# Kernel tuning notes

Measured on AMD Instinct MI355X. Metric: run time of the kernel, lower is better.

The kernel has to match this reference:

```python
import jax, jax.numpy as jnp
import numpy as np

BATCH = 256
B_TYPES = 32   # input capsule types
C_TYPES = 10   # output capsule types
H, W = 8, 8    # input spatial extent == kernel (output is 1x1)
POSE = 16      # capsule pose length (shape (16,1))
NUM_ITER = 3
EPS = 1e-8


def setup_inputs() -> dict:
    key = jax.random.key(0)
    k1, k2, k3 = jax.random.split(key, 3)
    input_caps_poses = jax.random.normal(k1, (BATCH, B_TYPES, H, W, POSE, 1), jnp.float32)
    input_caps_activations = jax.random.uniform(k2, (BATCH, B_TYPES, H, W), jnp.float32)
    # nn.init.normal_(std=0.1) on [B, kh, kw, C, os0, is0]
    weight = 0.1 * jax.random.normal(k3, (B_TYPES, H, W, C_TYPES, POSE, POSE), jnp.float32)
    # routing_bias initialized to 0.1: [C, oh, ow, os0, os1]
    routing_bias = jnp.full((C_TYPES, 1, 1, POSE, 1), 0.1, jnp.float32)
    return {
        "input_caps_poses": input_caps_poses,
        "input_caps_activations": input_caps_activations,
        "weight": weight,
        "routing_bias": routing_bias,
    }


def _squash(s):
    # Hinton squash: ||s||^2/(1+||s||^2) * s/||s||, norm over pose dims
    n2 = jnp.sum(s * s, axis=(-2, -1), keepdims=True)
    return (n2 / (1.0 + n2)) * s * jax.lax.rsqrt(n2 + EPS)


def reference(input_caps_poses, input_caps_activations, weight, routing_bias):
    b = input_caps_poses.shape[0]
    # votes[b,c,B,h,w,o,p] = sum_i W[B,h,w,c,o,i] * pose[b,B,h,w,i,p]
    votes = jnp.einsum('Bhwcoi,bBhwip->bcBhwop', weight, input_caps_poses)
    logits = jnp.zeros((b, C_TYPES, B_TYPES, H, W), votes.dtype)
    bias = routing_bias.reshape(1, C_TYPES, POSE, 1)
    v = None
    for it in range(NUM_ITER):
        # coupling coefficients: softmax over output capsule types
        c = jax.nn.softmax(logits, axis=1)                      # [b,C,B,h,w]
        # weighted sum of votes over all input capsules (B,h,w)
        s = jnp.einsum('bcBhw,bcBhwop->bcop', c, votes) + bias  # [b,C,16,1]
        v = _squash(s)
        if it < NUM_ITER - 1:
            # agreement: dot(vote, output pose)
            logits = logits + jnp.einsum('bcBhwop,bcop->bcBhw', votes, v)
    output_caps_poses = v[:, :, None, None, :, :]               # [b,C,1,1,16,1]
    output_caps_activations = jnp.sqrt(
        jnp.sum(v * v, axis=(-2, -1)) + EPS)[:, :, None, None]  # [b,C,1,1]
    return output_caps_poses, output_caps_activations
```

## Files before the change

### kernel.cpp

```cpp
#include <hip/hip_runtime.h>
#include <hip/hip_fp16.h>
#include <math.h>


typedef _Float16 f16;
typedef _Float16 f16x2 __attribute__((ext_vector_type(2)));
typedef _Float16 f16x4 __attribute__((ext_vector_type(4)));
typedef _Float16 f16x8 __attribute__((ext_vector_type(8)));
typedef __fp16   h16x2 __attribute__((ext_vector_type(2)));
typedef float f32x4 __attribute__((ext_vector_type(4)));

#define DPP_ADD(v, ctrl) ((v) + __int_as_float(__builtin_amdgcn_update_dpp( \
    0, __float_as_int(v), (ctrl), 0xF, 0xF, true)))

__device__ __forceinline__ f16x2 pk(float a, float b) {
    h16x2 t = __builtin_amdgcn_cvt_pkrtz(a, b);
    return __builtin_bit_cast(f16x2, t);
}

#if __has_builtin(__builtin_amdgcn_fdot2)
__device__ __forceinline__ float FDOT2(f16x2 a, f16x2 b, float c) {
    return __builtin_amdgcn_fdot2(__builtin_bit_cast(h16x2, a),
                                  __builtin_bit_cast(h16x2, b), c, false);
}
#else
__device__ __forceinline__ float FDOT2(f16x2 a, f16x2 b, float c) {
    return c + (float)a[0] * (float)b[0] + (float)a[1] * (float)b[1];
}
#endif

constexpr int WS_ROW = 28;
constexpr int XS_ROW = 76;

__device__ __forceinline__ float xorsum4(float v) {
    v += __shfl_xor(v, 16, 64);
    v += __shfl_xor(v, 32, 64);
    return v;
}

__device__ __forceinline__ f16x4 cvt4(float4 w) {
    f16x2 a = pk(w.x, w.y);
    f16x2 b = pk(w.z, w.w);
    f16x4 r; r[0] = a[0]; r[1] = a[1]; r[2] = b[0]; r[3] = b[1];
    return r;
}

template<int PASS>
__global__ __launch_bounds__(256)
void pass_k(const float* __restrict__ poses, const float* __restrict__ weight,
            const float* __restrict__ bias,
            const float* __restrict__ sp0, const float* __restrict__ sp1,
            float* __restrict__ s_dst)
{
    __shared__ f16 Ws[640 * WS_ROW];
    __shared__ f16 xs[64 * XS_ROW];

    const int tid  = threadIdx.x;
    const int blk  = blockIdx.x;
    const int ngrp = blk >> 2;
    const int b0   = (blk & 3) * 64;
    const int wave = tid >> 6;
    const int lane = tid & 63;
    const int q    = lane >> 4;
    const int lo   = lane & 15;
    const int wtb  = wave * 16;
    const int bg   = b0 + wtb;
    const int nl0  = q >> 1;
    const int iq   = (q & 1) * 8;

    f16x2 vsp[10][2];
    if (PASS >= 1) {
        const int rowb = (bg + lo) * 10;
        #pragma unroll
        for (int c = 0; c < 10; ++c) {
            float4 bb = *(const float4*)(bias + c * 16 + q * 4);
            float4 sa = *(const float4*)(sp0 + (size_t)(rowb + c) * 16 + q * 4);
            float t0 = sa.x + bb.x, t1 = sa.y + bb.y, t2 = sa.z + bb.z, t3 = sa.w + bb.w;
            float n2 = xorsum4(t0*t0 + t1*t1 + t2*t2 + t3*t3);
            float sc = n2 / (1.f + n2) * rsqrtf(n2 + 1e-8f);
            float v0 = sc*t0, v1 = sc*t1, v2 = sc*t2, v3 = sc*t3;
            if (PASS == 2) {
                float4 sb = *(const float4*)(sp1 + (size_t)(rowb + c) * 16 + q * 4);
                float u0 = sb.x + bb.x, u1 = sb.y + bb.y, u2 = sb.z + bb.z, u3 = sb.w + bb.w;
                float m2 = xorsum4(u0*u0 + u1*u1 + u2*u2 + u3*u3);
                float sc2 = m2 / (1.f + m2) * rsqrtf(m2 + 1e-8f);
                v0 += sc2*u0; v1 += sc2*u1; v2 += sc2*u2; v3 += sc2*u3;
            }
            vsp[c][0] = pk(v0, v1);
            vsp[c][1] = pk(v2, v3);
        }
    }

    float4 wreg[10];
    float4 xreg[4];
    const int b_loc = tid >> 2, part = tid & 3;

    auto load_iter = [&](int l) {
        const float* wp = weight + (size_t)(ngrp * 4 + l) * 10240;
        #pragma unroll
        for (int k = 0; k < 10; ++k) wreg[k] = ((const float4*)wp)[tid + k * 256];
        const float* xp = poses + (size_t)(b0 + b_loc) * 32768
                          + (size_t)(ngrp * 16 + l * 4 + part) * 16;
        #pragma unroll
        for (int j = 0; j < 4; ++j) xreg[j] = ((const float4*)xp)[j];
    };
    auto store_iter = [&]() {
        #pragma unroll
        for (int k = 0; k < 10; ++k) {
            const int f = tid + k * 256;
            *(f16x4*)&Ws[(f >> 2) * WS_ROW + (f & 3) * 4] = cvt4(wreg[k]);
        }
        f16* lp = xs + b_loc * XS_ROW + part * 16;
        #pragma unroll
        for (int j = 0; j < 4; ++j) *(f16x4*)&lp[j * 4] = cvt4(xreg[j]);
    };

    f32x4 acc[10];
    #pragma unroll
    for (int c = 0; c < 10; ++c) acc[c] = (f32x4){0.f, 0.f, 0.f, 0.f};

    f16x2 cf[10][2];

    load_iter(0);

    for (int l = 0; l < 4; ++l) {
        __syncthreads();
        store_iter();
        if (l + 1 < 4) load_iter(l + 1);
        __syncthreads();

        if (PASS >= 1) {
            float ce[10];
            #pragma unroll
            for (int n = 0; n < 4; ++n) {
                f16x4 bx = *(const f16x4*)&xs[(wtb + lo) * XS_ROW + n * 16 + q * 4];
                float lg[10];
                #pragma unroll
                for (int c = 0; c < 10; ++c) {
                    f16x4 aw = *(const f16x4*)&Ws[((n * 10 + c) * 16 + lo) * WS_ROW + q * 4];
                    f32x4 D = __builtin_amdgcn_mfma_f32_16x16x16f16(
                        aw, bx, (f32x4){0.f, 0.f, 0.f, 0.f}, 0, 0, 0);
                    float p = FDOT2(pk(D[0], D[1]), vsp[c][0], 0.f);
                    p = FDOT2(pk(D[2], D[3]), vsp[c][1], p);
                    lg[c] = xorsum4(p);
                }
                float m = lg[0];
                #pragma unroll
                for (int c = 1; c < 10; ++c) m = fmaxf(m, lg[c]);
                float sum = 0.f;
                #pragma unroll
                for (int c = 0; c < 10; ++c) { lg[c] = __expf(lg[c] - m); sum += lg[c]; }
                const float inv = 1.f / sum;
                if (n & 1) {
                    #pragma unroll
                    for (int c = 0; c < 10; ++c)
                        cf[c][n >> 1] = pk(ce[c], lg[c] * inv);
                } else {
                    #pragma unroll
                    for (int c = 0; c < 10; ++c) ce[c] = lg[c] * inv;
                }
            }
        }

        f16x8 xa[2];
        #pragma unroll
        for (int np = 0; np < 2; ++np) {
            const f16* p = &xs[(wtb + lo) * XS_ROW + (np * 2 + nl0) * 16 + iq];
            f16x4 x0 = *(const f16x4*)p;
            f16x4 x1 = *(const f16x4*)(p + 4);
            xa[np] = __builtin_shufflevector(x0, x1, 0, 1, 2, 3, 4, 5, 6, 7);
        }
        #pragma unroll
        for (int c = 0; c < 10; ++c) {
            #pragma unroll
            for (int np = 0; np < 2; ++np) {
                f16 ch;
                if (PASS == 0) {
                    ch = (f16)0.1f;
                } else {
                    union { f16x2 h; unsigned u; } cu; cu.h = cf[c][np];
                    unsigned hv = nl0 ? (cu.u >> 16) : (cu.u & 0xffffu);
                    union { unsigned short s; f16 h; } hu; hu.s = (unsigned short)hv;
                    ch = hu.h;
                }
                const int n_loc = np * 2 + nl0;
                const f16* wp_ = &Ws[((n_loc * 10 + c) * 16 + lo) * WS_ROW + iq];
                f16x4 w0 = *(const f16x4*)wp_;
                f16x4 w1 = *(const f16x4*)(wp_ + 4);
                f16x8 bw = __builtin_shufflevector(w0, w1, 0, 1, 2, 3, 4, 5, 6, 7);
                f16x8 av = xa[np] * ch;
                acc[c] = __builtin_amdgcn_mfma_f32_16x16x32_f16(av, bw, acc[c], 0, 0, 0);
            }
        }
    }

    #pragma unroll
    for (int c = 0; c < 10; ++c) {
        float* sp = s_dst + ((size_t)(bg + q * 4) * 10 + c) * 16 + lo;
        unsafeAtomicAdd(sp + 0 * 160, acc[c][0]);
        unsafeAtomicAdd(sp + 1 * 160, acc[c][1]);
        unsafeAtomicAdd(sp + 2 * 160, acc[c][2]);
        unsafeAtomicAdd(sp + 3 * 160, acc[c][3]);
    }
}

__global__ __launch_bounds__(256)
void epi_k(const float* __restrict__ s2, const float* __restrict__ bias,
           float* __restrict__ out)
{
    const int t = blockIdx.x * 256 + threadIdx.x;
    if (t >= 2560) return;
    const int c = t % 10;
    const float* sp = s2 + (size_t)t * 16;
    const float* bp = bias + c * 16;
    float sv[16];
    float n2 = 0.f;
    #pragma unroll
    for (int o = 0; o < 16; ++o) { float v = sp[o] + bp[o]; sv[o] = v; n2 += v * v; }
    const float scale = n2 / (1.f + n2) * rsqrtf(n2 + 1e-8f);
    float a2 = 0.f;
    #pragma unroll
    for (int o = 0; o < 16; ++o) {
        float v = scale * sv[o];
        out[(size_t)t * 16 + o] = v;
        a2 += v * v;
    }
    out[40960 + t] = sqrtf(a2 + 1e-8f);
}

extern "C" void kernel_launch(void* const* d_in, const int* in_sizes, int n_in,
                              void* d_out, int out_size, void* d_ws, size_t ws_size,
                              hipStream_t stream)
{
    const float* poses  = (const float*)d_in[0];
    const float* weight = (const float*)d_in[2];
    const float* bias   = (const float*)d_in[3];
    float* out = (float*)d_out;
    float* s0 = (float*)d_ws;
    float* s1 = s0 + 40960;
    float* s2 = s1 + 40960;

    (void)hipMemsetAsync(d_ws, 0, 3 * 40960 * sizeof(float), stream);

    pass_k<0><<<512, 256, 0, stream>>>(poses, weight, bias, nullptr, nullptr, s0);
    pass_k<1><<<512, 256, 0, stream>>>(poses, weight, bias, s0, nullptr, s1);
    pass_k<2><<<512, 256, 0, stream>>>(poses, weight, bias, s0, s1, s2);
    epi_k<<<10, 256, 0, stream>>>(s2, bias, out);
}
```

Baseline: 204.7 us.

## Reuse vote MFMA results for weighted sum instead of second MFMA pass

The per-position vote tiles computed by the 16x16x16 MFMA are now kept in registers and accumulated directly, each scaled by its coupling coefficient with FMAs. This replaces the separate 16x16x32 MFMA pass that recomputed the same products from shared memory. The agreement reduction packs two logits into an f16x2 before the cross-lane shuffle, halving shuffle count. Launch bounds now request 2 blocks per CU. Risks are reduced precision in the fp16 logit reduction, a changed atomic write layout, and higher register pressure from holding 10 f32x4 vote tiles.

```diff
diff --git a/kernel.cpp b/kernel.cpp
--- a/kernel.cpp
+++ b/kernel.cpp
@@ -6,12 +6,8 @@
 typedef _Float16 f16;
 typedef _Float16 f16x2 __attribute__((ext_vector_type(2)));
 typedef _Float16 f16x4 __attribute__((ext_vector_type(4)));
-typedef _Float16 f16x8 __attribute__((ext_vector_type(8)));
 typedef __fp16   h16x2 __attribute__((ext_vector_type(2)));
 typedef float f32x4 __attribute__((ext_vector_type(4)));
-
-#define DPP_ADD(v, ctrl) ((v) + __int_as_float(__builtin_amdgcn_update_dpp( \
-    0, __float_as_int(v), (ctrl), 0xF, 0xF, true)))
 
 __device__ __forceinline__ f16x2 pk(float a, float b) {
     h16x2 t = __builtin_amdgcn_cvt_pkrtz(a, b);
@@ -35,6 +31,14 @@
 __device__ __forceinline__ float xorsum4(float v) {
     v += __shfl_xor(v, 16, 64);
     v += __shfl_xor(v, 32, 64);
+    return v;
+}
+
+__device__ __forceinline__ f16x2 xorsum4h(f16x2 v) {
+    union { f16x2 h; int i; } u;
+    union { int i; f16x2 h; } w;
+    u.h = v; w.i = __shfl_xor(u.i, 16, 64); v = v + w.h;
+    u.h = v; w.i = __shfl_xor(u.i, 32, 64); v = v + w.h;
     return v;
 }
 
@@ -46,7 +50,7 @@
 }
 
 template<int PASS>
-__global__ __launch_bounds__(256)
+__global__ __launch_bounds__(256, 2)
 void pass_k(const float* __restrict__ poses, const float* __restrict__ weight,
             const float* __restrict__ bias,
             const float* __restrict__ sp0, const float* __restrict__ sp1,
@@ -65,8 +69,6 @@
     const int lo   = lane & 15;
     const int wtb  = wave * 16;
     const int bg   = b0 + wtb;
-    const int nl0  = q >> 1;
-    const int iq   = (q & 1) * 8;
 
     f16x2 vsp[10][2];
     if (PASS >= 1) {
@@ -119,8 +121,6 @@
     #pragma unroll
     for (int c = 0; c < 10; ++c) acc[c] = (f32x4){0.f, 0.f, 0.f, 0.f};
 
-    f16x2 cf[10][2];
-
     load_iter(0);
 
     for (int l = 0; l < 4; ++l) {
@@ -129,20 +129,30 @@
         if (l + 1 < 4) load_iter(l + 1);
         __syncthreads();
 
-        if (PASS >= 1) {
-            float ce[10];
+        #pragma unroll
+        for (int n = 0; n < 4; ++n) {
+            f16x4 bx = *(const f16x4*)&xs[(wtb + lo) * XS_ROW + n * 16 + q * 4];
+            f32x4 V[10];
             #pragma unroll
-            for (int n = 0; n < 4; ++n) {
-                f16x4 bx = *(const f16x4*)&xs[(wtb + lo) * XS_ROW + n * 16 + q * 4];
+            for (int c = 0; c < 10; ++c) {
+                f16x4 aw = *(const f16x4*)&Ws[((n * 10 + c) * 16 + lo) * WS_ROW + q * 4];
+                V[c] = __builtin_amdgcn_mfma_f32_16x16x16f16(
+                    aw, bx, (f32x4){0.f, 0.f, 0.f, 0.f}, 0, 0, 0);
+            }
+
+            float cfv[10];
+            if (PASS >= 1) {
                 float lg[10];
                 #pragma unroll
-                for (int c = 0; c < 10; ++c) {
-                    f16x4 aw = *(const f16x4*)&Ws[((n * 10 + c) * 16 + lo) * WS_ROW + q * 4];
-                    f32x4 D = __builtin_amdgcn_mfma_f32_16x16x16f16(
-                        aw, bx, (f32x4){0.f, 0.f, 0.f, 0.f}, 0, 0, 0);
-                    float p = FDOT2(pk(D[0], D[1]), vsp[c][0], 0.f);
-                    p = FDOT2(pk(D[2], D[3]), vsp[c][1], p);
-                    lg[c] = xorsum4(p);
+                for (int cp = 0; cp < 5; ++cp) {
+                    const int c0 = cp * 2, c1 = cp * 2 + 1;
+                    float p0 = FDOT2(pk(V[c0][0], V[c0][1]), vsp[c0][0], 0.f);
+                    p0 = FDOT2(pk(V[c0][2], V[c0][3]), vsp[c0][1], p0);
+                    float p1 = FDOT2(pk(V[c1][0], V[c1][1]), vsp[c1][0], 0.f);
+                    p1 = FDOT2(pk(V[c1][2], V[c1][3]), vsp[c1][1], p1);
+                    f16x2 pr = xorsum4h(pk(p0, p1));
+                    lg[c0] = (float)pr[0];
+                    lg[c1] = (float)pr[1];
                 }
                 float m = lg[0];
                 #pragma unroll
@@ -151,56 +161,28 @@
                 #pragma unroll
                 for (int c = 0; c < 10; ++c) { lg[c] = __expf(lg[c] - m); sum += lg[c]; }
                 const float inv = 1.f / sum;
-                if (n & 1) {
-                    #pragma unroll
-                    for (int c = 0; c < 10; ++c)
-                        cf[c][n >> 1] = pk(ce[c], lg[c] * inv);
-                } else {
-                    #pragma unroll
-                    for (int c = 0; c < 10; ++c) ce[c] = lg[c] * inv;
-                }
+                #pragma unroll
+                for (int c = 0; c < 10; ++c) cfv[c] = lg[c] * inv;
+            }
+
+            #pragma unroll
+            for (int c = 0; c < 10; ++c) {
+                const float w = (PASS == 0) ? 1.f : cfv[c];
+                #pragma unroll
+                for (int r = 0; r < 4; ++r)
+                    acc[c][r] = fmaf(w, V[c][r], acc[c][r]);
             }
         }
-
-        f16x8 xa[2];
-        #pragma unroll
-        for (int np = 0; np < 2; ++np) {
-            const f16* p = &xs[(wtb + lo) * XS_ROW + (np * 2 + nl0) * 16 + iq];
-            f16x4 x0 = *(const f16x4*)p;
-            f16x4 x1 = *(const f16x4*)(p + 4);
-            xa[np] = __builtin_shufflevector(x0, x1, 0, 1, 2, 3, 4, 5, 6, 7);
-        }
-        #pragma unroll
-        for (int c = 0; c < 10; ++c) {
-            #pragma unroll
-            for (int np = 0; np < 2; ++np) {
-                f16 ch;
-                if (PASS == 0) {
-                    ch = (f16)0.1f;
-                } else {
-                    union { f16x2 h; unsigned u; } cu; cu.h = cf[c][np];
-                    unsigned hv = nl0 ? (cu.u >> 16) : (cu.u & 0xffffu);
-                    union { unsigned short s; f16 h; } hu; hu.s = (unsigned short)hv;
-                    ch = hu.h;
-                }
-                const int n_loc = np * 2 + nl0;
-                const f16* wp_ = &Ws[((n_loc * 10 + c) * 16 + lo) * WS_ROW + iq];
-                f16x4 w0 = *(const f16x4*)wp_;
-                f16x4 w1 = *(const f16x4*)(wp_ + 4);
-                f16x8 bw = __builtin_shufflevector(w0, w1, 0, 1, 2, 3, 4, 5, 6, 7);
-                f16x8 av = xa[np] * ch;
-                acc[c] = __builtin_amdgcn_mfma_f32_16x16x32_f16(av, bw, acc[c], 0, 0, 0);
-            }
-        }
-    }
-
+    }
+
+    const float fs = (PASS == 0) ? 0.1f : 1.f;
     #pragma unroll
     for (int c = 0; c < 10; ++c) {
-        float* sp = s_dst + ((size_t)(bg + q * 4) * 10 + c) * 16 + lo;
-        unsafeAtomicAdd(sp + 0 * 160, acc[c][0]);
-        unsafeAtomicAdd(sp + 1 * 160, acc[c][1]);
-        unsafeAtomicAdd(sp + 2 * 160, acc[c][2]);
-        unsafeAtomicAdd(sp + 3 * 160, acc[c][3]);
+        float* sp = s_dst + ((size_t)(bg + lo) * 10 + c) * 16 + q * 4;
+        unsafeAtomicAdd(sp + 0, fs * acc[c][0]);
+        unsafeAtomicAdd(sp + 1, fs * acc[c][1]);
+        unsafeAtomicAdd(sp + 2, fs * acc[c][2]);
+        unsafeAtomicAdd(sp + 3, fs * acc[c][3]);
     }
 }
 
```

Measured after the change: 480.4 us. 135% more time.
